# Performance work log

Hardware: AMD Instinct MI355X
Metric: run time of the kernel (lower is better)

The kernel has to match this reference:

```python
import math
import jax, jax.numpy as jnp
import numpy as np

SINKHORN_ITERS = 5
SINKHORN_REG = 1.0
D_MODEL, KDIM, VDIM = 512, 512, 512
B, T, N = 8, 2048, 2048


def _xavier(key, shape):
    fan_in, fan_out = shape[0], shape[1]
    bound = math.sqrt(6.0 / (fan_in + fan_out))
    return jax.random.uniform(key, shape, jnp.float32, -bound, bound)


def setup_inputs() -> dict:
    key = jax.random.key(0)
    kq, kk, kv, kQ, kK, kV = jax.random.split(key, 6)
    return {
        "q": jax.random.normal(kq, (T, D_MODEL), jnp.float32),
        "k": jax.random.normal(kk, (B, N, KDIM), jnp.float32),
        "v": jax.random.normal(kv, (B, N, VDIM), jnp.float32),
        "Q": _xavier(kQ, (D_MODEL, D_MODEL)),
        "K": _xavier(kK, (KDIM, D_MODEL)),
        "V": _xavier(kV, (VDIM, D_MODEL)),
    }


def _cdist(q, k):
    # q: [T, d], k: [B, N, d] -> Euclidean distances [B, T, N]
    q2 = jnp.sum(q * q, axis=-1)            # [T]
    k2 = jnp.sum(k * k, axis=-1)            # [B, N]
    qk = jnp.einsum('td,bnd->btn', q, k)    # [B, T, N]
    sq = q2[None, :, None] + k2[:, None, :] - 2.0 * qk
    return jnp.sqrt(jnp.maximum(sq, 0.0))


def _sinkhorn(q, k, iters, reg):
    costs = _cdist(q, k)                    # [B, T, N]
    Kmat = -costs / reg
    num_params = k.shape[1]
    num_tokens = q.shape[0]
    log_a = -jnp.log(jnp.float32(num_params))
    log_b = jnp.float32(0.0)
    u = jnp.zeros((k.shape[0], 1, num_params), Kmat.dtype)
    v = jnp.zeros((k.shape[0], num_tokens, 1), Kmat.dtype)
    for _ in range(iters):
        u = log_a - jax.scipy.special.logsumexp(Kmat + v, axis=1, keepdims=True)
        v = log_b - jax.scipy.special.logsumexp(Kmat + u, axis=2, keepdims=True)
    return jnp.exp(Kmat + u + v)


def reference(q, k, v, Q, K, V):
    qp = q @ Q                               # [T, d_model]
    kp = k @ K                               # [B, N, d_model]
    vp = v @ V                               # [B, N, d_model]
    pi = _sinkhorn(qp, kp, SINKHORN_ITERS, SINKHORN_REG)  # [B, T, N]
    return jnp.einsum('btn,bnd->btd', pi, vp)              # [B, T, d_model]
```

## Files before the change

### kernel.cpp

```cpp
#include <hip/hip_runtime.h>
#include <math.h>

#define TT 2048
#define NP 2048
#define BB 8
#define DD 512

#define LOG_A (-7.6246189861593985f)
#define CC 30.0f
#define E30 1.0686475e13f
#define K0U 5.2180055e9f

typedef __attribute__((ext_vector_type(8))) _Float16 f16x8;
typedef __attribute__((ext_vector_type(4))) _Float16 f16x4;
typedef __attribute__((ext_vector_type(4))) float f32x4;

#define MFMA_F16(a, b, c)  __builtin_amdgcn_mfma_f32_16x16x32_f16((a), (b), (c), 0, 0, 0)

__device__ __forceinline__ float f16u2f(unsigned short u) {
    union { unsigned short s; _Float16 h; } v; v.s = u;
    return (float)v.h;
}

__device__ __forceinline__ void gload16(const void* g, void* l) {
    __builtin_amdgcn_global_load_lds(
        (const __attribute__((address_space(1))) void*)g,
        (__attribute__((address_space(3))) void*)l, 16, 0, 0);
}

__device__ __forceinline__ void frag_step_f16(
    const _Float16* sA, const _Float16* sB,
    int lane, int wm, int wn, f32x4 acc[4][4])
{
    const int sb = (lane >> 4) << 11;
    const int rl = (lane & 15) << 4;
    f16x8 a[4], b[4];
    #pragma unroll
    for (int i = 0; i < 4; ++i) {
        a[i] = *(const f16x8*)((const char*)sA + sb + ((wm + i * 16) << 4) + rl);
        b[i] = *(const f16x8*)((const char*)sB + sb + ((wn + i * 16) << 4) + rl);
    }
    #pragma unroll
    for (int i = 0; i < 4; ++i)
        #pragma unroll
        for (int j = 0; j < 4; ++j)
            acc[i][j] = MFMA_F16(a[i], b[j], acc[i][j]);
}

__device__ __forceinline__ void zero_acc(f32x4 acc[4][4]) {
    #pragma unroll
    for (int i = 0; i < 4; ++i)
        #pragma unroll
        for (int j = 0; j < 4; ++j)
            acc[i][j] = (f32x4){0.f, 0.f, 0.f, 0.f};
}

__device__ __forceinline__ void store_plain(
    float* C, int N, int row0, int col0, int lane, int wm, int wn, f32x4 acc[4][4])
{
    #pragma unroll
    for (int i = 0; i < 4; ++i)
        #pragma unroll
        for (int j = 0; j < 4; ++j) {
            int colg = col0 + wn + j * 16 + (lane & 15);
            int rowb = row0 + wm + i * 16 + ((lane >> 4) << 2);
            #pragma unroll
            for (int r = 0; r < 4; ++r)
                C[(size_t)(rowb + r) * N + colg] = acc[i][j][r];
        }
}

__global__ __launch_bounds__(256) void transpose3_f16(
    const float* __restrict__ X0, const float* __restrict__ X1,
    const float* __restrict__ X2, _Float16* __restrict__ o0,
    _Float16* __restrict__ o1, _Float16* __restrict__ o2)
{
    const int z = blockIdx.z;
    const float* Xb = (z == 0) ? X0 : (z == 1) ? X1 : X2;
    _Float16* ob = (z == 0) ? o0 : (z == 1) ? o1 : o2;
    __shared__ float t[64][65];
    const int bx = blockIdx.x * 64;
    const int by = blockIdx.y * 64;
    const int tx = threadIdx.x & 63, ty = threadIdx.x >> 6;
    #pragma unroll
    for (int r = ty; r < 64; r += 4)
        t[r][tx] = Xb[(size_t)(by + r) * 512 + bx + tx];
    __syncthreads();
    #pragma unroll
    for (int r = ty; r < 64; r += 4)
        ob[(size_t)(bx + r) * 512 + by + tx] = (_Float16)t[tx][r];
}

__global__ __launch_bounds__(256) void gemm_projqk_f16(
    const float* __restrict__ Aq, const float* __restrict__ Ak,
    const _Float16* __restrict__ Btq, const _Float16* __restrict__ Btk,
    _Float16* __restrict__ C)
{
    const int by = blockIdx.y;
    const bool isq = (by < 16);
    const float* A = isq ? Aq : Ak;
    const _Float16* Bt = isq ? Btq : Btk;
    const int arow0 = isq ? by * 128 : (by - 16) * 128;
    const int crow0 = by * 128;
    const int col0 = blockIdx.x * 128;

    __shared__ __attribute__((aligned(16))) _Float16 sA[4096], sB[4096];
    const int tid = threadIdx.x;
    const int lane = tid & 63;
    const int wm = ((tid >> 7) & 1) * 64;
    const int wn = ((tid >> 6) & 1) * 64;
    f32x4 acc[4][4];
    zero_acc(acc);

    for (int k0 = 0; k0 < DD; k0 += 32) {
        __syncthreads();
        #pragma unroll
        for (int q = 0; q < 2; ++q) {
            int o = (tid + (q << 8)) << 4;
            int s = o >> 11;
            int r = (o & 2047) >> 4;
            gload16(Bt + (size_t)(col0 + r) * DD + k0 + s * 8, (char*)sB + o);
            const float* src = A + (size_t)(arow0 + r) * DD + k0 + s * 8;
            float4 f0 = *(const float4*)src;
            float4 f1 = *(const float4*)(src + 4);
            _Float16 hs[8] = {(_Float16)f0.x, (_Float16)f0.y,
                              (_Float16)f0.z, (_Float16)f0.w,
                              (_Float16)f1.x, (_Float16)f1.y,
                              (_Float16)f1.z, (_Float16)f1.w};
            *(f16x8*)((char*)sA + o) = *(f16x8*)hs;
        }
        __syncthreads();
        frag_step_f16(sA, sB, lane, wm, wn, acc);
    }
    #pragma unroll
    for (int i = 0; i < 4; ++i)
        #pragma unroll
        for (int j = 0; j < 4; ++j) {
            int colg = col0 + wn + j * 16 + (lane & 15);
            int rowb = crow0 + wm + i * 16 + ((lane >> 4) << 2);
            #pragma unroll
            for (int r = 0; r < 4; ++r)
                C[(size_t)(rowb + r) * DD + colg] = (_Float16)acc[i][j][r];
        }
}

__global__ __launch_bounds__(256) void gemm_projv_f16(
    const float* __restrict__ A, const _Float16* __restrict__ Bt,
    _Float16* __restrict__ C)
{
    __shared__ __attribute__((aligned(16))) _Float16 sA[4096], sB[4096];
    const int tid = threadIdx.x;
    const int lane = tid & 63;
    const int row0 = blockIdx.y * 128;
    const int col0 = blockIdx.x * 128;
    const int wm = ((tid >> 7) & 1) * 64;
    const int wn = ((tid >> 6) & 1) * 64;
    f32x4 acc[4][4];
    zero_acc(acc);

    for (int k0 = 0; k0 < DD; k0 += 32) {
        __syncthreads();
        #pragma unroll
        for (int q = 0; q < 2; ++q) {
            int o = (tid + (q << 8)) << 4;
            int s = o >> 11;
            int r = (o & 2047) >> 4;
            gload16(Bt + (size_t)(col0 + r) * DD + k0 + s * 8, (char*)sB + o);
            const float* src = A + (size_t)(row0 + r) * DD + k0 + s * 8;
            float4 f0 = *(const float4*)src;
            float4 f1 = *(const float4*)(src + 4);
            _Float16 hs[8] = {(_Float16)f0.x, (_Float16)f0.y,
                              (_Float16)f0.z, (_Float16)f0.w,
                              (_Float16)f1.x, (_Float16)f1.y,
                              (_Float16)f1.z, (_Float16)f1.w};
            *(f16x8*)((char*)sA + o) = *(f16x8*)hs;
        }
        __syncthreads();
        frag_step_f16(sA, sB, lane, wm, wn, acc);
    }
    #pragma unroll
    for (int i = 0; i < 4; ++i)
        #pragma unroll
        for (int j = 0; j < 4; ++j) {
            int colg = col0 + wn + j * 16 + (lane & 15);
            int rowb = row0 + wm + i * 16 + ((lane >> 4) << 2);
            int b = rowb >> 11;
            int n0 = rowb & (NP - 1);
            _Float16 h4[4];
            #pragma unroll
            for (int r = 0; r < 4; ++r) h4[r] = (_Float16)acc[i][j][r];
            *(f16x4*)(C + (size_t)b * DD * NP + (size_t)colg * NP + n0) =
                *(f16x4*)h4;
        }
}

__global__ __launch_bounds__(256) void rownorm_f16(
    const _Float16* __restrict__ X, float* __restrict__ o, int rows)
{
    int w = blockIdx.x * 4 + (threadIdx.x >> 6);
    int lane = threadIdx.x & 63;
    if (w >= rows) return;
    f16x8 v = *(const f16x8*)(X + (size_t)w * DD + lane * 8);
    float s = 0.f;
    #pragma unroll
    for (int j = 0; j < 8; ++j) {
        float x = (float)v[j];
        s = fmaf(x, x, s);
    }
    #pragma unroll
    for (int off = 32; off; off >>= 1) s += __shfl_down(s, off, 64);
    if (lane == 0) o[w] = s;
}

__global__ __launch_bounds__(256) void gemm_cost_f16(
    const _Float16* __restrict__ A, const _Float16* __restrict__ B,
    const float* __restrict__ q2, const float* __restrict__ k2,
    _Float16* __restrict__ E)
{
    const int bid = blockIdx.x;
    const int sid = ((bid & 7) << 8) | (bid >> 3);
    const int b  = sid >> 8;
    const int by = (sid >> 4) & 15;
    const int bx = sid & 15;

    const _Float16* Bb = B + (size_t)b * NP * DD;
    const float* k2b = k2 + (size_t)b * NP;
    _Float16* Cb = E + (size_t)b * TT * NP;

    __shared__ __attribute__((aligned(16))) _Float16 sA[3][4096], sB[3][4096];
    const int tid = threadIdx.x;
    const int lane = tid & 63;
    const int row0 = by * 128;
    const int col0 = bx * 128;
    const int wm = ((tid >> 7) & 1) * 64;
    const int wn = ((tid >> 6) & 1) * 64;
    f32x4 acc[4][4];
    zero_acc(acc);

    auto STAGE = [&](int buf, int k0) {
        #pragma unroll
        for (int q = 0; q < 2; ++q) {
            int o = (tid + (q << 8)) << 4;
            int s = o >> 11;
            int r = (o & 2047) >> 4;
            gload16(A + (size_t)(row0 + r) * DD + k0 + s * 8, (char*)&sA[buf][0] + o);
            gload16(Bb + (size_t)(col0 + r) * DD + k0 + s * 8, (char*)&sB[buf][0] + o);
        }
    };

    STAGE(0, 0);
    STAGE(1, 32);

    #pragma unroll
    for (int s = 0; s < 14; ++s) {
        asm volatile("s_waitcnt vmcnt(4)" ::: "memory");
        __builtin_amdgcn_s_barrier();
        __builtin_amdgcn_sched_barrier(0);
        STAGE((s + 2) % 3, (s + 2) * 32);
        frag_step_f16(&sA[s % 3][0], &sB[s % 3][0], lane, wm, wn, acc);
    }
    asm volatile("s_waitcnt vmcnt(4)" ::: "memory");
    __builtin_amdgcn_s_barrier();
    __builtin_amdgcn_sched_barrier(0);
    frag_step_f16(&sA[2][0], &sB[2][0], lane, wm, wn, acc);
    asm volatile("s_waitcnt vmcnt(0)" ::: "memory");
    __builtin_amdgcn_s_barrier();
    __builtin_amdgcn_sched_barrier(0);
    frag_step_f16(&sA[0][0], &sB[0][0], lane, wm, wn, acc);

    #pragma unroll
    for (int i = 0; i < 4; ++i)
        #pragma unroll
        for (int j = 0; j < 4; ++j) {
            int colg = col0 + wn + j * 16 + (lane & 15);
            float k2v = k2b[colg];
            int rowb = row0 + wm + i * 16 + ((lane >> 4) << 2);
            #pragma unroll
            for (int r = 0; r < 4; ++r) {
                float sq = q2[rowb + r] + k2v - 2.f * acc[i][j][r];
                float dist = sqrtf(fmaxf(sq, 0.f));
                float e = fminf(__expf(CC - dist), 60000.f);
                Cb[(size_t)(rowb + r) * NP + colg] = (_Float16)e;
            }
        }
}

template<bool FIRST>
__global__ __launch_bounds__(256) void sink_fused(
    const _Float16* __restrict__ E, const float* __restrict__ U,
    float* __restrict__ ps)
{
    const int b = blockIdx.y;
    const int t0 = blockIdx.x * 32;
    const int tid = threadIdx.x;
    const int n0 = tid * 8;
    const _Float16* Eb = E + ((size_t)b * TT + t0) * NP;

    float u8[8];
    if (!FIRST) {
        float4 a = *(const float4*)(U + (size_t)b * NP + n0);
        float4 c = *(const float4*)(U + (size_t)b * NP + n0 + 4);
        u8[0] = a.x; u8[1] = a.y; u8[2] = a.z; u8[3] = a.w;
        u8[4] = c.x; u8[5] = c.y; u8[6] = c.z; u8[7] = c.w;
    }

    float cs[8] = {0.f, 0.f, 0.f, 0.f, 0.f, 0.f, 0.f, 0.f};
    __shared__ float red[8][256];
    __shared__ float yy[8];

    #pragma unroll
    for (int g = 0; g < 4; ++g) {
        uint4 ev[8];
        #pragma unroll
        for (int r = 0; r < 8; ++r)
            ev[r] = *(const uint4*)(Eb + (size_t)(g * 8 + r) * NP + n0);

        if (!FIRST) {
            #pragma unroll
            for (int r = 0; r < 8; ++r) {
                float d = 0.f;
                d = fmaf(f16u2f((unsigned short)(ev[r].x & 0xFFFFu)), u8[0], d);
                d = fmaf(f16u2f((unsigned short)(ev[r].x >> 16)),     u8[1], d);
                d = fmaf(f16u2f((unsigned short)(ev[r].y & 0xFFFFu)), u8[2], d);
                d = fmaf(f16u2f((unsigned short)(ev[r].y >> 16)),     u8[3], d);
                d = fmaf(f16u2f((unsigned short)(ev[r].z & 0xFFFFu)), u8[4], d);
                d = fmaf(f16u2f((unsigned short)(ev[r].z >> 16)),     u8[5], d);
                d = fmaf(f16u2f((unsigned short)(ev[r].w & 0xFFFFu)), u8[6], d);
                d = fmaf(f16u2f((unsigned short)(ev[r].w >> 16)),     u8[7], d);
                red[r][tid] = d;
            }
            __syncthreads();
            {
                int w = tid >> 6, lane = tid & 63;
                #pragma unroll
                for (int rr = 0; rr < 2; ++rr) {
                    int r = w * 2 + rr;
                    float s = red[r][lane] + red[r][lane + 64] +
                              red[r][lane + 128] + red[r][lane + 192];
                    #pragma unroll
                    for (int off = 32; off; off >>= 1)
                        s += __shfl_down(s, off, 64);
                    if (lane == 0) yy[r] = E30 / s;
                }
            }
            __syncthreads();
            #pragma unroll
            for (int r = 0; r < 8; ++r) {
                float yv = yy[r];
                cs[0] = fmaf(f16u2f((unsigned short)(ev[r].x & 0xFFFFu)), yv, cs[0]);
                cs[1] = fmaf(f16u2f((unsigned short)(ev[r].x >> 16)),     yv, cs[1]);
                cs[2] = fmaf(f16u2f((unsigned short)(ev[r].y & 0xFFFFu)), yv, cs[2]);
                cs[3] = fmaf(f16u2f((unsigned short)(ev[r].y >> 16)),     yv, cs[3]);
                cs[4] = fmaf(f16u2f((unsigned short)(ev[r].z & 0xFFFFu)), yv, cs[4]);
                cs[5] = fmaf(f16u2f((unsigned short)(ev[r].z >> 16)),     yv, cs[5]);
                cs[6] = fmaf(f16u2f((unsigned short)(ev[r].w & 0xFFFFu)), yv, cs[6]);
                cs[7] = fmaf(f16u2f((unsigned short)(ev[r].w >> 16)),     yv, cs[7]);
            }
            __syncthreads();
        } else {
            #pragma unroll
            for (int r = 0; r < 8; ++r) {
                cs[0] += f16u2f((unsigned short)(ev[r].x & 0xFFFFu));
                cs[1] += f16u2f((unsigned short)(ev[r].x >> 16));
                cs[2] += f16u2f((unsigned short)(ev[r].y & 0xFFFFu));
                cs[3] += f16u2f((unsigned short)(ev[r].y >> 16));
                cs[4] += f16u2f((unsigned short)(ev[r].z & 0xFFFFu));
                cs[5] += f16u2f((unsigned short)(ev[r].z >> 16));
                cs[6] += f16u2f((unsigned short)(ev[r].w & 0xFFFFu));
                cs[7] += f16u2f((unsigned short)(ev[r].w >> 16));
            }
        }
    }

    size_t o = ((size_t)b * 64 + blockIdx.x) * NP + n0;
    *(float4*)(ps + o)     = make_float4(cs[0], cs[1], cs[2], cs[3]);
    *(float4*)(ps + o + 4) = make_float4(cs[4], cs[5], cs[6], cs[7]);
}

__global__ __launch_bounds__(256) void u_combine(
    const float* __restrict__ ps, float* __restrict__ U)
{
    int gid = blockIdx.x * 256 + threadIdx.x;
    int b = gid >> 11;
    int n = gid & (NP - 1);
    float S = 0.f;
    #pragma unroll 8
    for (int c = 0; c < 64; ++c)
        S += ps[((size_t)b * 64 + c) * NP + n];
    U[gid] = K0U / S;
}

__global__ __launch_bounds__(256) void v_final(
    const _Float16* __restrict__ E, const float* __restrict__ U,
    _Float16* __restrict__ P)
{
    const int b = blockIdx.y;
    const int t = blockIdx.x;
    const uint4* Eb = (const uint4*)(E + ((size_t)b * TT + t) * NP);
    const float* Ub = U + (size_t)b * NP;
    const int tid = threadIdx.x;

    uint4 w = Eb[tid];
    const int n0 = tid * 8;
    float4 u0 = *(const float4*)(Ub + n0);
    float4 u1 = *(const float4*)(Ub + n0 + 4);
    float ev[8];
    ev[0] = f16u2f((unsigned short)(w.x & 0xFFFFu));
    ev[1] = f16u2f((unsigned short)(w.x >> 16));
    ev[2] = f16u2f((unsigned short)(w.y & 0xFFFFu));
    ev[3] = f16u2f((unsigned short)(w.y >> 16));
    ev[4] = f16u2f((unsigned short)(w.z & 0xFFFFu));
    ev[5] = f16u2f((unsigned short)(w.z >> 16));
    ev[6] = f16u2f((unsigned short)(w.w & 0xFFFFu));
    ev[7] = f16u2f((unsigned short)(w.w >> 16));
    float uv[8] = {u0.x, u0.y, u0.z, u0.w, u1.x, u1.y, u1.z, u1.w};

    float s = 0.f;
    #pragma unroll
    for (int j = 0; j < 8; ++j) s = fmaf(ev[j], uv[j], s);
    #pragma unroll
    for (int off = 32; off; off >>= 1) s += __shfl_down(s, off, 64);

    __shared__ float sw[4];
    __shared__ float Sall;
    if ((tid & 63) == 0) sw[tid >> 6] = s;
    __syncthreads();
    if (tid == 0) Sall = sw[0] + sw[1] + sw[2] + sw[3];
    __syncthreads();
    float invS = 1.0f / Sall;
    _Float16 hp[8];
    #pragma unroll
    for (int j = 0; j < 8; ++j)
        hp[j] = (_Float16)(ev[j] * uv[j] * invS);
    *(f16x8*)(P + ((size_t)b * TT + t) * NP + n0) = *(f16x8*)hp;
}

__global__ __launch_bounds__(256) void gemm_pi_f16(
    const _Float16* __restrict__ P, const _Float16* __restrict__ B,
    float* __restrict__ out)
{
    const int bid = blockIdx.x;
    const int sid = ((bid & 7) << 6) | (bid >> 3);
    const int b  = sid >> 6;
    const int by = (sid >> 2) & 15;
    const int bx = sid & 3;

    const _Float16* Pb = P + (size_t)b * TT * NP;
    const _Float16* Bb = B + (size_t)b * DD * NP;
    float* Cb = out + (size_t)b * TT * DD;

    __shared__ __attribute__((aligned(16))) _Float16 sA[2][4096], sB[2][4096];
    const int tid = threadIdx.x;
    const int lane = tid & 63;
    const int row0 = by * 128;
    const int col0 = bx * 128;
    const int wm = ((tid >> 7) & 1) * 64;
    const int wn = ((tid >> 6) & 1) * 64;
    f32x4 acc[4][4];
    zero_acc(acc);

    auto STAGE = [&](int buf, int k0) {
        #pragma unroll
        for (int q = 0; q < 2; ++q) {
            int o = (tid + (q << 8)) << 4;
            int s = o >> 11;
            int r = (o & 2047) >> 4;
            gload16(Pb + (size_t)(row0 + r) * NP + k0 + s * 8, (char*)&sA[buf][0] + o);
            gload16(Bb + (size_t)(col0 + r) * NP + k0 + s * 8, (char*)&sB[buf][0] + o);
        }
    };

    STAGE(0, 0);
    __syncthreads();
    int cur = 0;
    for (int k0 = 0; k0 < NP; k0 += 32) {
        if (k0 + 32 < NP) STAGE(cur ^ 1, k0 + 32);
        frag_step_f16(&sA[cur][0], &sB[cur][0], lane, wm, wn, acc);
        __syncthreads();
        cur ^= 1;
    }
    store_plain(Cb, DD, row0, col0, lane, wm, wn, acc);
}

extern "C" void kernel_launch(void* const* d_in, const int* in_sizes, int n_in,
                              void* d_out, int out_size, void* d_ws, size_t ws_size,
                              hipStream_t stream)
{
    const float* q  = (const float*)d_in[0];
    const float* k  = (const float*)d_in[1];
    const float* v  = (const float*)d_in[2];
    const float* Qw = (const float*)d_in[3];
    const float* Kw = (const float*)d_in[4];
    const float* Vw = (const float*)d_in[5];
    float* out = (float*)d_out;

    char* base = (char*)d_ws;
    _Float16* E16 = (_Float16*)base;
    char* p2 = base + (size_t)BB * TT * NP * 2;
    _Float16* P   = (_Float16*)p2; p2 += (size_t)BB * TT * NP * 2;
    _Float16* qpf = (_Float16*)p2; p2 += (size_t)TT * DD * 2;
    _Float16* kpf = (_Float16*)p2; p2 += (size_t)BB * NP * DD * 2;
    _Float16* vpt = (_Float16*)p2; p2 += (size_t)BB * DD * NP * 2;
    float* q2 = (float*)p2; p2 += (size_t)TT * 4;
    float* k2 = (float*)p2; p2 += (size_t)BB * NP * 4;
    float* U  = (float*)p2; p2 += (size_t)BB * NP * 4;
    float* ps = (float*)p2; p2 += (size_t)BB * 64 * NP * 4;

    _Float16* wq = (_Float16*)base;
    _Float16* wk = wq + 262144;
    _Float16* wv = wk + 262144;

    dim3 blk(256);

    transpose3_f16<<<dim3(8, 8, 3), blk, 0, stream>>>(Qw, Kw, Vw, wq, wk, wv);

    gemm_projqk_f16<<<dim3(4, 144, 1), blk, 0, stream>>>(q, k, wq, wk, qpf);
    gemm_projv_f16<<<dim3(4, 128, 1), blk, 0, stream>>>(v, wv, vpt);

    rownorm_f16<<<dim3((TT + BB * NP) / 4), blk, 0, stream>>>(qpf, q2, TT + BB * NP);

    gemm_cost_f16<<<dim3(2048), blk, 0, stream>>>(qpf, kpf, q2, k2, E16);

    sink_fused<true><<<dim3(TT / 32, BB), blk, 0, stream>>>(E16, U, ps);
    u_combine<<<dim3(BB * NP / 256), blk, 0, stream>>>(ps, U);
    for (int it = 0; it < 4; ++it) {
        sink_fused<false><<<dim3(TT / 32, BB), blk, 0, stream>>>(E16, U, ps);
        u_combine<<<dim3(BB * NP / 256), blk, 0, stream>>>(ps, U);
    }
    v_final<<<dim3(TT, BB), blk, 0, stream>>>(E16, U, P);

    gemm_pi_f16<<<dim3(512), blk, 0, stream>>>(P, vpt, out);
}
```

Baseline: 392.5 us.

## Fuse first Sinkhorn column-sum into cost GEMM epilogue; triple-buffer pi GEMM

The cost GEMM epilogue now accumulates per-column sums of the exponentiated costs and writes 16 partial sums per batch. This replaces the first sink_fused pass, which re-read the whole 64 MB fp16 E matrix. The final pi GEMM also moves from a double-buffered loop with __syncthreads to a 3-stage pipeline with vmcnt waits, matching the cost GEMM. The trade-offs are extra epilogue work and shuffles in the cost GEMM, more LDS in the pi GEMM, and column sums now taken from fp32 values before fp16 rounding.

```diff
diff --git a/kernel.cpp b/kernel.cpp
--- a/kernel.cpp
+++ b/kernel.cpp
@@ -215,7 +215,7 @@
 __global__ __launch_bounds__(256) void gemm_cost_f16(
     const _Float16* __restrict__ A, const _Float16* __restrict__ B,
     const float* __restrict__ q2, const float* __restrict__ k2,
-    _Float16* __restrict__ E)
+    _Float16* __restrict__ E, float* __restrict__ ps16)
 {
     const int bid = blockIdx.x;
     const int sid = ((bid & 7) << 8) | (bid >> 3);
@@ -228,6 +228,7 @@
     _Float16* Cb = E + (size_t)b * TT * NP;
 
     __shared__ __attribute__((aligned(16))) _Float16 sA[3][4096], sB[3][4096];
+    __shared__ float colbuf[2][128];
     const int tid = threadIdx.x;
     const int lane = tid & 63;
     const int row0 = by * 128;
@@ -250,7 +251,6 @@
 
     STAGE(0, 0);
     STAGE(1, 32);
-
     #pragma unroll
     for (int s = 0; s < 14; ++s) {
         asm volatile("s_waitcnt vmcnt(4)" ::: "memory");
@@ -268,6 +268,7 @@
     __builtin_amdgcn_sched_barrier(0);
     frag_step_f16(&sA[0][0], &sB[0][0], lane, wm, wn, acc);
 
+    float csum[4] = {0.f, 0.f, 0.f, 0.f};
     #pragma unroll
     for (int i = 0; i < 4; ++i)
         #pragma unroll
@@ -280,12 +281,24 @@
                 float sq = q2[rowb + r] + k2v - 2.f * acc[i][j][r];
                 float dist = sqrtf(fmaxf(sq, 0.f));
                 float e = fminf(__expf(CC - dist), 60000.f);
+                csum[j] += e;
                 Cb[(size_t)(rowb + r) * NP + colg] = (_Float16)e;
             }
         }
-}
-
-template<bool FIRST>
+    #pragma unroll
+    for (int j = 0; j < 4; ++j) {
+        float s = csum[j];
+        s += __shfl_down(s, 32, 64);
+        s += __shfl_down(s, 16, 64);
+        if (lane < 16)
+            colbuf[wm >> 6][wn + j * 16 + lane] = s;
+    }
+    __syncthreads();
+    if (tid < 128)
+        ps16[((size_t)b * 16 + by) * NP + col0 + tid] =
+            colbuf[0][tid] + colbuf[1][tid];
+}
+
 __global__ __launch_bounds__(256) void sink_fused(
     const _Float16* __restrict__ E, const float* __restrict__ U,
     float* __restrict__ ps)
@@ -297,7 +310,7 @@
     const _Float16* Eb = E + ((size_t)b * TT + t0) * NP;
 
     float u8[8];
-    if (!FIRST) {
+    {
         float4 a = *(const float4*)(U + (size_t)b * NP + n0);
         float4 c = *(const float4*)(U + (size_t)b * NP + n0 + 4);
         u8[0] = a.x; u8[1] = a.y; u8[2] = a.z; u8[3] = a.w;
@@ -315,61 +328,47 @@
         for (int r = 0; r < 8; ++r)
             ev[r] = *(const uint4*)(Eb + (size_t)(g * 8 + r) * NP + n0);
 
-        if (!FIRST) {
+        #pragma unroll
+        for (int r = 0; r < 8; ++r) {
+            float d = 0.f;
+            d = fmaf(f16u2f((unsigned short)(ev[r].x & 0xFFFFu)), u8[0], d);
+            d = fmaf(f16u2f((unsigned short)(ev[r].x >> 16)),     u8[1], d);
+            d = fmaf(f16u2f((unsigned short)(ev[r].y & 0xFFFFu)), u8[2], d);
+            d = fmaf(f16u2f((unsigned short)(ev[r].y >> 16)),     u8[3], d);
+            d = fmaf(f16u2f((unsigned short)(ev[r].z & 0xFFFFu)), u8[4], d);
+            d = fmaf(f16u2f((unsigned short)(ev[r].z >> 16)),     u8[5], d);
+            d = fmaf(f16u2f((unsigned short)(ev[r].w & 0xFFFFu)), u8[6], d);
+            d = fmaf(f16u2f((unsigned short)(ev[r].w >> 16)),     u8[7], d);
+            red[r][tid] = d;
+        }
+        __syncthreads();
+        {
+            int w = tid >> 6, lane = tid & 63;
             #pragma unroll
-            for (int r = 0; r < 8; ++r) {
-                float d = 0.f;
-                d = fmaf(f16u2f((unsigned short)(ev[r].x & 0xFFFFu)), u8[0], d);
-                d = fmaf(f16u2f((unsigned short)(ev[r].x >> 16)),     u8[1], d);
-                d = fmaf(f16u2f((unsigned short)(ev[r].y & 0xFFFFu)), u8[2], d);
-                d = fmaf(f16u2f((unsigned short)(ev[r].y >> 16)),     u8[3], d);
-                d = fmaf(f16u2f((unsigned short)(ev[r].z & 0xFFFFu)), u8[4], d);
-                d = fmaf(f16u2f((unsigned short)(ev[r].z >> 16)),     u8[5], d);
-                d = fmaf(f16u2f((unsigned short)(ev[r].w & 0xFFFFu)), u8[6], d);
-                d = fmaf(f16u2f((unsigned short)(ev[r].w >> 16)),     u8[7], d);
-                red[r][tid] = d;
+            for (int rr = 0; rr < 2; ++rr) {
+                int r = w * 2 + rr;
+                float s = red[r][lane] + red[r][lane + 64] +
+                          red[r][lane + 128] + red[r][lane + 192];
+                #pragma unroll
+                for (int off = 32; off; off >>= 1)
+                    s += __shfl_down(s, off, 64);
+                if (lane == 0) yy[r] = E30 / s;
             }
-            __syncthreads();
-            {
-                int w = tid >> 6, lane = tid & 63;
-                #pragma unroll
-                for (int rr = 0; rr < 2; ++rr) {
-                    int r = w * 2 + rr;
-                    float s = red[r][lane] + red[r][lane + 64] +
-                              red[r][lane + 128] + red[r][lane + 192];
-                    #pragma unroll
-                    for (int off = 32; off; off >>= 1)
-                        s += __shfl_down(s, off, 64);
-                    if (lane == 0) yy[r] = E30 / s;
-                }
-            }
-            __syncthreads();
-            #pragma unroll
-            for (int r = 0; r < 8; ++r) {
-                float yv = yy[r];
-                cs[0] = fmaf(f16u2f((unsigned short)(ev[r].x & 0xFFFFu)), yv, cs[0]);
-                cs[1] = fmaf(f16u2f((unsigned short)(ev[r].x >> 16)),     yv, cs[1]);
-                cs[2] = fmaf(f16u2f((unsigned short)(ev[r].y & 0xFFFFu)), yv, cs[2]);
-                cs[3] = fmaf(f16u2f((unsigned short)(ev[r].y >> 16)),     yv, cs[3]);
-                cs[4] = fmaf(f16u2f((unsigned short)(ev[r].z & 0xFFFFu)), yv, cs[4]);
-                cs[5] = fmaf(f16u2f((unsigned short)(ev[r].z >> 16)),     yv, cs[5]);
-                cs[6] = fmaf(f16u2f((unsigned short)(ev[r].w & 0xFFFFu)), yv, cs[6]);
-                cs[7] = fmaf(f16u2f((unsigned short)(ev[r].w >> 16)),     yv, cs[7]);
-            }
-            __syncthreads();
-        } else {
-            #pragma unroll
-            for (int r = 0; r < 8; ++r) {
-                cs[0] += f16u2f((unsigned short)(ev[r].x & 0xFFFFu));
-                cs[1] += f16u2f((unsigned short)(ev[r].x >> 16));
-                cs[2] += f16u2f((unsigned short)(ev[r].y & 0xFFFFu));
-                cs[3] += f16u2f((unsigned short)(ev[r].y >> 16));
-                cs[4] += f16u2f((unsigned short)(ev[r].z & 0xFFFFu));
-                cs[5] += f16u2f((unsigned short)(ev[r].z >> 16));
-                cs[6] += f16u2f((unsigned short)(ev[r].w & 0xFFFFu));
-                cs[7] += f16u2f((unsigned short)(ev[r].w >> 16));
-            }
-        }
+        }
+        __syncthreads();
+        #pragma unroll
+        for (int r = 0; r < 8; ++r) {
+            float yv = yy[r];
+            cs[0] = fmaf(f16u2f((unsigned short)(ev[r].x & 0xFFFFu)), yv, cs[0]);
+            cs[1] = fmaf(f16u2f((unsigned short)(ev[r].x >> 16)),     yv, cs[1]);
+            cs[2] = fmaf(f16u2f((unsigned short)(ev[r].y & 0xFFFFu)), yv, cs[2]);
+            cs[3] = fmaf(f16u2f((unsigned short)(ev[r].y >> 16)),     yv, cs[3]);
+            cs[4] = fmaf(f16u2f((unsigned short)(ev[r].z & 0xFFFFu)), yv, cs[4]);
+            cs[5] = fmaf(f16u2f((unsigned short)(ev[r].z >> 16)),     yv, cs[5]);
+            cs[6] = fmaf(f16u2f((unsigned short)(ev[r].w & 0xFFFFu)), yv, cs[6]);
+            cs[7] = fmaf(f16u2f((unsigned short)(ev[r].w >> 16)),     yv, cs[7]);
+        }
+        __syncthreads();
     }
 
     size_t o = ((size_t)b * 64 + blockIdx.x) * NP + n0;
@@ -377,6 +376,7 @@
     *(float4*)(ps + o + 4) = make_float4(cs[4], cs[5], cs[6], cs[7]);
 }
 
+template<int NCH>
 __global__ __launch_bounds__(256) void u_combine(
     const float* __restrict__ ps, float* __restrict__ U)
 {
@@ -385,8 +385,8 @@
     int n = gid & (NP - 1);
     float S = 0.f;
     #pragma unroll 8
-    for (int c = 0; c < 64; ++c)
-        S += ps[((size_t)b * 64 + c) * NP + n];
+    for (int c = 0; c < NCH; ++c)
+        S += ps[((size_t)b * NCH + c) * NP + n];
     U[gid] = K0U / S;
 }
 
@@ -449,7 +449,7 @@
     const _Float16* Bb = B + (size_t)b * DD * NP;
     float* Cb = out + (size_t)b * TT * DD;
 
-    __shared__ __attribute__((aligned(16))) _Float16 sA[2][4096], sB[2][4096];
+    __shared__ __attribute__((aligned(16))) _Float16 sA[3][4096], sB[3][4096];
     const int tid = threadIdx.x;
     const int lane = tid & 63;
     const int row0 = by * 128;
@@ -470,15 +470,32 @@
         }
     };
 
+    #define PI_STEP(BUFC, BUFS, KS)                               \
+        asm volatile("s_waitcnt vmcnt(4)" ::: "memory");          \
+        __builtin_amdgcn_s_barrier();                             \
+        __builtin_amdgcn_sched_barrier(0);                        \
+        STAGE(BUFS, (KS) * 32);                                   \
+        frag_step_f16(&sA[BUFC][0], &sB[BUFC][0], lane, wm, wn, acc);
+
     STAGE(0, 0);
-    __syncthreads();
-    int cur = 0;
-    for (int k0 = 0; k0 < NP; k0 += 32) {
-        if (k0 + 32 < NP) STAGE(cur ^ 1, k0 + 32);
-        frag_step_f16(&sA[cur][0], &sB[cur][0], lane, wm, wn, acc);
-        __syncthreads();
-        cur ^= 1;
-    }
+    STAGE(1, 32);
+    for (int s3 = 0; s3 < 60; s3 += 3) {
+        PI_STEP(0, 2, s3 + 2)
+        PI_STEP(1, 0, s3 + 3)
+        PI_STEP(2, 1, s3 + 4)
+    }
+    PI_STEP(0, 2, 62)
+    PI_STEP(1, 0, 63)
+    asm volatile("s_waitcnt vmcnt(4)" ::: "memory");
+    __builtin_amdgcn_s_barrier();
+    __builtin_amdgcn_sched_barrier(0);
+    frag_step_f16(&sA[2][0], &sB[2][0], lane, wm, wn, acc);
+    asm volatile("s_waitcnt vmcnt(0)" ::: "memory");
+    __builtin_amdgcn_s_barrier();
+    __builtin_amdgcn_sched_barrier(0);
+    frag_step_f16(&sA[0][0], &sB[0][0], lane, wm, wn, acc);
+    #undef PI_STEP
+
     store_plain(Cb, DD, row0, col0, lane, wm, wn, acc);
 }
 
@@ -519,13 +536,12 @@
 
     rownorm_f16<<<dim3((TT + BB * NP) / 4), blk, 0, stream>>>(qpf, q2, TT + BB * NP);
 
-    gemm_cost_f16<<<dim3(2048), blk, 0, stream>>>(qpf, kpf, q2, k2, E16);
-
-    sink_fused<true><<<dim3(TT / 32, BB), blk, 0, stream>>>(E16, U, ps);
-    u_combine<<<dim3(BB * NP / 256), blk, 0, stream>>>(ps, U);
+    gemm_cost_f16<<<dim3(2048), blk, 0, stream>>>(qpf, kpf, q2, k2, E16, ps);
+
+    u_combine<16><<<dim3(BB * NP / 256), blk, 0, stream>>>(ps, U);
     for (int it = 0; it < 4; ++it) {
-        sink_fused<false><<<dim3(TT / 32, BB), blk, 0, stream>>>(E16, U, ps);
-        u_combine<<<dim3(BB * NP / 256), blk, 0, stream>>>(ps, U);
+        sink_fused<<<dim3(TT / 32, BB), blk, 0, stream>>>(E16, U, ps);
+        u_combine<64><<<dim3(BB * NP / 256), blk, 0, stream>>>(ps, U);
     }
     v_final<<<dim3(TT, BB), blk, 0, stream>>>(E16, U, P);
 
```

Measured after the change: 384.1 us. 1.02x faster.
